# Optimization experiments

Measured on AMD Instinct MI355X. Metric: run time of the kernel, lower is better.

## Reference

```python
import jax, jax.numpy as jnp
import numpy as np

B, T, D = 2, 1024, 1024   # batch, seq, d_model
E, F = 8, 4096            # n_experts, expert hidden (4*d_model)


def setup_inputs() -> dict:
    key = jax.random.key(0)
    k1, k2, k3, k4, k5 = jax.random.split(key, 5)
    x = jax.random.normal(k1, (B, T, D), dtype=jnp.float32)
    token_mask = jax.random.randint(k2, (B, T), 0, 2).astype(jnp.int32)
    router_w = jax.random.normal(k3, (E, D), dtype=jnp.float32) * (1.0 / np.sqrt(D))
    w1 = jax.random.normal(k4, (E, D, F), dtype=jnp.float32) * (1.0 / np.sqrt(D))
    w2 = jax.random.normal(k5, (E, F, D), dtype=jnp.float32) * (1.0 / np.sqrt(F))
    return {"x": x, "token_mask": token_mask, "router_w": router_w, "w1": w1, "w2": w2}


def reference(x, token_mask, router_w, w1, w2):
    b, t, d = x.shape
    n_exp = router_w.shape[0]
    xf = x.reshape(b * t, d)                       # [N, D]
    # top-1 router
    logits = xf @ router_w.T                       # [N, E]
    probs = jax.nn.softmax(logits, axis=-1)
    expert_idx = jnp.argmax(probs, axis=-1)        # [N]
    gate = jnp.take_along_axis(probs, expert_idx[:, None], axis=1)[:, 0]  # [N]
    # expert FFNs: each token routed to exactly one expert (dense masked combine)
    y = jnp.zeros_like(xf)
    for e in range(n_exp):
        he = jnp.maximum(xf @ w1[e], 0.0) @ w2[e]  # [N, D]
        y = jnp.where(expert_idx[:, None] == e, he, y)
    # gate scaling + token masking (masked rows stay exactly zero,
    # matching torch's zero-init y_flat_all + index_copy_)
    mask = token_mask.reshape(b * t).astype(x.dtype)
    out = y * (gate * mask)[:, None]
    return out.reshape(b, t, d)
```

## Files before the change

kernel.cpp:

```cpp
#include <hip/hip_runtime.h>
#include <hip/hip_bf16.h>

#define NTOK 2048
#define DM 1024
#define NEXP 8
#define FFN 4096
#define BM 64
#define BN 64
#define BK 64
#define ASTR 72
#define MT1 8
#define G2_SPLIT 4

typedef __bf16 bf16x8 __attribute__((ext_vector_type(8)));
typedef __bf16 bf16x4 __attribute__((ext_vector_type(4)));
typedef float f32x4 __attribute__((ext_vector_type(4)));

__device__ __forceinline__ bf16x8 zero8() {
  bf16x8 z;
#pragma unroll
  for (int j = 0; j < 8; j++) z[j] = (__bf16)0.f;
  return z;
}

__device__ __forceinline__ void xpose4(float v[4], int quad) {
  const bool b0 = quad & 1;
  const bool b1 = (quad & 2) != 0;
  float t;
  t = __shfl_xor(b0 ? v[0] : v[1], 16, 64); if (b0) v[0] = t; else v[1] = t;
  t = __shfl_xor(b0 ? v[2] : v[3], 16, 64); if (b0) v[2] = t; else v[3] = t;
  t = __shfl_xor(b1 ? v[0] : v[2], 32, 64); if (b1) v[0] = t; else v[2] = t;
  t = __shfl_xor(b1 ? v[1] : v[3], 32, 64); if (b1) v[1] = t; else v[3] = t;
}

__device__ __forceinline__ bf16x8 readB(const char* BsB, int row, int kh, int quad) {
  return *(const bf16x8*)(BsB + row * 144 +
                          ((((kh << 2) + quad) ^ (row >> 3)) << 4));
}

#define STOREB(bb, v4, it) do {                                          \
    float vv[4] = {(v4).x, (v4).y, (v4).z, (v4).w};                      \
    xpose4(vv, quad);                                                    \
    bf16x4 o;                                                            \
    o[0] = (__bf16)vv[0]; o[1] = (__bf16)vv[1];                          \
    o[2] = (__bf16)vv[2]; o[3] = (__bf16)vv[3];                          \
    *(bf16x4*)((bb) + (((((it) << 1) + (w >> 1)) ^ rsw) << 4)) = o;      \
  } while (0)

__global__ __launch_bounds__(256) void router_gather(
    const float* __restrict__ x, const int* __restrict__ mask,
    const float* __restrict__ rw, int* __restrict__ counts,
    int* __restrict__ tlist, float* __restrict__ gateE,
    __bf16* __restrict__ xg)
{
  int wid = threadIdx.x >> 6, lane = threadIdx.x & 63;
  int t = blockIdx.x * 4 + wid;

  const float* xr = x + (size_t)t * DM;
  float xv[16];
#pragma unroll
  for (int i = 0; i < 4; i++) {
    const float4 v = *(const float4*)(xr + lane * 16 + i * 4);
    xv[i * 4 + 0] = v.x; xv[i * 4 + 1] = v.y;
    xv[i * 4 + 2] = v.z; xv[i * 4 + 3] = v.w;
  }

  float acc[NEXP];
#pragma unroll
  for (int e = 0; e < NEXP; e++) {
    float a = 0.f;
    const float* rwe = rw + e * DM + lane * 16;
#pragma unroll
    for (int i = 0; i < 4; i++) {
      const float4 r = *(const float4*)(rwe + i * 4);
      a += xv[i*4+0]*r.x + xv[i*4+1]*r.y + xv[i*4+2]*r.z + xv[i*4+3]*r.w;
    }
    acc[e] = a;
  }
#pragma unroll
  for (int e = 0; e < NEXP; e++)
#pragma unroll
    for (int s = 1; s < 64; s <<= 1) acc[e] += __shfl_xor(acc[e], s, 64);

  int pack = -1;
  if (lane == 0 && mask[t] != 0) {
    float m = acc[0]; int am = 0;
#pragma unroll
    for (int e = 1; e < NEXP; e++) if (acc[e] > m) { m = acc[e]; am = e; }
    float s = 0.f;
#pragma unroll
    for (int e = 0; e < NEXP; e++) s += __expf(acc[e] - m);
    int slot = atomicAdd(&counts[am], 1);
    tlist[am * NTOK + slot] = t;
    gateE[am * NTOK + slot] = 1.0f / s;
    pack = am * NTOK + slot;
  }
  pack = __shfl(pack, 0, 64);
  if (pack >= 0) {
    __bf16* dst = xg + (size_t)pack * DM + lane * 16;
    bf16x8 o0, o1;
#pragma unroll
    for (int j = 0; j < 8; j++) {
      o0[j] = (__bf16)xv[j];
      o1[j] = (__bf16)xv[8 + j];
    }
    *(bf16x8*)dst = o0;
    *(bf16x8*)(dst + 8) = o1;
  }
}

__global__ __launch_bounds__(256) void moe_gemm1(
    const __bf16* __restrict__ xg, const float* __restrict__ w1,
    const int* __restrict__ counts, const int* __restrict__ tlist,
    __bf16* __restrict__ h)
{
  int bx = blockIdx.x;
  int nt = bx & 63, mt = (bx >> 6) & (MT1 - 1), e = bx >> 9;
  int cnt = counts[e];
  if (mt * BM >= cnt) return;
  int n0 = nt * BN;

  __shared__ __bf16 As[BM][ASTR];
  __shared__ char   Bs[64 * 144];
  __shared__ int    toks[BM];

  int tid = threadIdx.x, lane = tid & 63, w = tid >> 6;
  int wm = w >> 1, wn = w & 1;
  int r16 = lane & 15, quad = lane >> 4;
  int rsw = r16 >> 1;
  char* bb = Bs + ((r16 << 2) + quad) * 144 + ((w & 1) << 3);

  const __bf16* xge = xg + (size_t)e * NTOK * DM;
  const float*  w1e = w1 + (size_t)e * DM * FFN;

  int ar = tid >> 2;
  int ak = (tid & 3) << 4;
  const float* bptr = w1e + (size_t)(w * 4 + quad) * FFN + n0 + (r16 << 2);

  bf16x8 a0r, a1r;
  float4 br0, br1, br2, br3;

#define LOADG1(kb) do {                                                   \
    a0r = av ? *(const bf16x8*)(aptr + (kb))     : zero8();               \
    a1r = av ? *(const bf16x8*)(aptr + (kb) + 8) : zero8();               \
    br0 = *(const float4*)(bptr + (size_t)((kb) +  0) * FFN);             \
    br1 = *(const float4*)(bptr + (size_t)((kb) + 16) * FFN);             \
    br2 = *(const float4*)(bptr + (size_t)((kb) + 32) * FFN);             \
    br3 = *(const float4*)(bptr + (size_t)((kb) + 48) * FFN);             \
  } while (0)

  for (int m0 = mt * BM; m0 < cnt; m0 += MT1 * BM) {
    bool av = (m0 + ar) < cnt;
    const __bf16* aptr = xge + (size_t)(m0 + ar) * DM + ak;

    f32x4 acc[2][2] = {};
    LOADG1(0);
    const int T = DM / BK;
    for (int t = 0; t < T; t++) {
      *(bf16x8*)&As[ar][ak]     = a0r;
      *(bf16x8*)&As[ar][ak + 8] = a1r;
      STOREB(bb, br0, 0); STOREB(bb, br1, 1); STOREB(bb, br2, 2); STOREB(bb, br3, 3);
      __syncthreads();
      if (t + 1 < T) LOADG1((t + 1) * BK);
#pragma unroll
      for (int kh = 0; kh < 2; kh++) {
        int ks = kh * 32 + (quad << 3);
        bf16x8 aA = *(const bf16x8*)&As[wm * 32 + r16][ks];
        bf16x8 aB = *(const bf16x8*)&As[wm * 32 + 16 + r16][ks];
        bf16x8 bA = readB(Bs, wn * 32 + r16, kh, quad);
        bf16x8 bB = readB(Bs, wn * 32 + 16 + r16, kh, quad);
        acc[0][0] = __builtin_amdgcn_mfma_f32_16x16x32_bf16(aA, bA, acc[0][0], 0, 0, 0);
        acc[0][1] = __builtin_amdgcn_mfma_f32_16x16x32_bf16(aA, bB, acc[0][1], 0, 0, 0);
        acc[1][0] = __builtin_amdgcn_mfma_f32_16x16x32_bf16(aB, bA, acc[1][0], 0, 0, 0);
        acc[1][1] = __builtin_amdgcn_mfma_f32_16x16x32_bf16(aB, bB, acc[1][1], 0, 0, 0);
      }
      __syncthreads();
    }

    if (tid < BM) toks[tid] = (m0 + tid < cnt) ? tlist[e * NTOK + m0 + tid] : -1;
    __syncthreads();

#pragma unroll
    for (int mf = 0; mf < 2; mf++) {
#pragma unroll
      for (int i = 0; i < 4; i++) {
        int row = wm * 32 + mf * 16 + (quad << 2) + i;
        int tok = toks[row];
        if (tok >= 0) {
          __bf16* hp = h + (size_t)tok * FFN + n0 + wn * 32 + r16;
          hp[0]  = (__bf16)fmaxf(acc[mf][0][i], 0.f);
          hp[16] = (__bf16)fmaxf(acc[mf][1][i], 0.f);
        }
      }
    }
    __syncthreads();
  }
#undef LOADG1
}

__global__ __launch_bounds__(256) void moe_gemm2(
    const __bf16* __restrict__ h, const float* __restrict__ w2,
    const int* __restrict__ counts, const int* __restrict__ tlist,
    const float* __restrict__ gateE, float* __restrict__ out)
{
  int bx = blockIdx.x;
  int nt = bx & 15, mt = (bx >> 4) & (MT1 - 1), e = (bx >> 7) & 7, sp = bx >> 10;
  int cnt = counts[e];
  if (mt * BM >= cnt) return;
  int n0 = nt * BN;
  int ksp = sp * (FFN / G2_SPLIT);

  __shared__ __bf16 As[BM][ASTR];
  __shared__ char   Bs[64 * 144];
  __shared__ int    toks[BM];
  __shared__ float  gts[BM];

  int tid = threadIdx.x, lane = tid & 63, w = tid >> 6;
  int wm = w >> 1, wn = w & 1;
  int r16 = lane & 15, quad = lane >> 4;
  int rsw = r16 >> 1;
  char* bb = Bs + ((r16 << 2) + quad) * 144 + ((w & 1) << 3);

  const float* w2e = w2 + (size_t)e * FFN * DM;
  int ar = tid >> 2;
  int ak = (tid & 3) << 4;
  const float* bptr = w2e + (size_t)(ksp + w * 4 + quad) * DM + n0 + (r16 << 2);

  bf16x8 a0r, a1r;
  float4 br0, br1, br2, br3;

#define LOADG2(kb) do {                                                   \
    a0r = av ? *(const bf16x8*)(aptr + (kb))     : zero8();               \
    a1r = av ? *(const bf16x8*)(aptr + (kb) + 8) : zero8();               \
    br0 = *(const float4*)(bptr + (size_t)((kb) +  0) * DM);              \
    br1 = *(const float4*)(bptr + (size_t)((kb) + 16) * DM);              \
    br2 = *(const float4*)(bptr + (size_t)((kb) + 32) * DM);              \
    br3 = *(const float4*)(bptr + (size_t)((kb) + 48) * DM);              \
  } while (0)

  for (int m0 = mt * BM; m0 < cnt; m0 += MT1 * BM) {
    if (tid < BM) {
      bool v = (m0 + tid) < cnt;
      toks[tid] = v ? tlist[e * NTOK + m0 + tid] : -1;
      gts[tid]  = v ? gateE[e * NTOK + m0 + tid] : 0.f;
    }
    __syncthreads();

    int tok0 = toks[ar];
    bool av = tok0 >= 0;
    const __bf16* aptr = h + (size_t)(av ? tok0 : 0) * FFN + ksp + ak;

    f32x4 acc[2][2] = {};
    LOADG2(0);
    const int T = (FFN / G2_SPLIT) / BK;
    for (int t = 0; t < T; t++) {
      *(bf16x8*)&As[ar][ak]     = a0r;
      *(bf16x8*)&As[ar][ak + 8] = a1r;
      STOREB(bb, br0, 0); STOREB(bb, br1, 1); STOREB(bb, br2, 2); STOREB(bb, br3, 3);
      __syncthreads();
      if (t + 1 < T) LOADG2((t + 1) * BK);
#pragma unroll
      for (int kh = 0; kh < 2; kh++) {
        int ks = kh * 32 + (quad << 3);
        bf16x8 aA = *(const bf16x8*)&As[wm * 32 + r16][ks];
        bf16x8 aB = *(const bf16x8*)&As[wm * 32 + 16 + r16][ks];
        bf16x8 bA = readB(Bs, wn * 32 + r16, kh, quad);
        bf16x8 bB = readB(Bs, wn * 32 + 16 + r16, kh, quad);
        acc[0][0] = __builtin_amdgcn_mfma_f32_16x16x32_bf16(aA, bA, acc[0][0], 0, 0, 0);
        acc[0][1] = __builtin_amdgcn_mfma_f32_16x16x32_bf16(aA, bB, acc[0][1], 0, 0, 0);
        acc[1][0] = __builtin_amdgcn_mfma_f32_16x16x32_bf16(aB, bA, acc[1][0], 0, 0, 0);
        acc[1][1] = __builtin_amdgcn_mfma_f32_16x16x32_bf16(aB, bB, acc[1][1], 0, 0, 0);
      }
      __syncthreads();
    }

#pragma unroll
    for (int mf = 0; mf < 2; mf++) {
#pragma unroll
      for (int i = 0; i < 4; i++) {
        int row = wm * 32 + mf * 16 + (quad << 2) + i;
        int tok = toks[row];
        if (tok >= 0) {
          float g = gts[row];
          float* op = out + (size_t)tok * DM + n0 + wn * 32 + r16;
          __hip_atomic_fetch_add(op, acc[mf][0][i] * g,
                                 __ATOMIC_RELAXED, __HIP_MEMORY_SCOPE_AGENT);
          __hip_atomic_fetch_add(op + 16, acc[mf][1][i] * g,
                                 __ATOMIC_RELAXED, __HIP_MEMORY_SCOPE_AGENT);
        }
      }
    }
    __syncthreads();
  }
#undef LOADG2
}

extern "C" void kernel_launch(void* const* d_in, const int* in_sizes, int n_in,
                              void* d_out, int out_size, void* d_ws, size_t ws_size,
                              hipStream_t stream) {
  const float* x    = (const float*)d_in[0];
  const int*   mask = (const int*)d_in[1];
  const float* rw   = (const float*)d_in[2];
  const float* w1   = (const float*)d_in[3];
  const float* w2   = (const float*)d_in[4];
  float* out = (float*)d_out;

  char* ws = (char*)d_ws;
  int*    counts = (int*)ws;
  int*    tlist  = (int*)(ws + 1024);
  float*  gateE  = (float*)(ws + 1024 + 65536);
  __bf16* xg     = (__bf16*)(ws + 132096);
  __bf16* h      = (__bf16*)(ws + 132096 +
                             (size_t)NEXP * NTOK * DM * 2);

  hipMemsetAsync(counts, 0, 1024, stream);
  hipMemsetAsync(out, 0, (size_t)out_size * sizeof(float), stream);

  router_gather<<<NTOK / 4, 256, 0, stream>>>(x, mask, rw, counts, tlist, gateE, xg);
  moe_gemm1<<<NEXP * MT1 * (FFN / BN), 256, 0, stream>>>(xg, w1, counts, tlist, h);
  moe_gemm2<<<G2_SPLIT * NEXP * MT1 * (DM / BN), 256, 0, stream>>>(
      h, w2, counts, tlist, gateE, out);
}
```

Baseline: 134.2 us.

## Double-buffer global prefetch and halve M-tile block count in MoE GEMMs

Both expert GEMMs now hold two register stages of global loads, so the tile for step t+2 is fetched while step t is stored to LDS and computed. Each kernel is unrolled by two over a fixed 16-step K loop. The number of M-tile slots per expert drops from 8 to 4, so each block loops over more row tiles and fewer blocks reload the same weight tile. Launch bounds now request 4 blocks per CU. The extra staging registers raise register pressure, and fewer blocks can reduce parallelism for experts that receive many tokens.

```diff
diff --git a/kernel.cpp b/kernel.cpp
--- a/kernel.cpp
+++ b/kernel.cpp
@@ -9,7 +9,7 @@
 #define BN 64
 #define BK 64
 #define ASTR 72
-#define MT1 8
+#define MTS 4
 #define G2_SPLIT 4
 
 typedef __bf16 bf16x8 __attribute__((ext_vector_type(8)));
@@ -109,13 +109,13 @@
   }
 }
 
-__global__ __launch_bounds__(256) void moe_gemm1(
+__global__ __launch_bounds__(256, 4) void moe_gemm1(
     const __bf16* __restrict__ xg, const float* __restrict__ w1,
     const int* __restrict__ counts, const int* __restrict__ tlist,
     __bf16* __restrict__ h)
 {
   int bx = blockIdx.x;
-  int nt = bx & 63, mt = (bx >> 6) & (MT1 - 1), e = bx >> 9;
+  int nt = bx & 63, mt = (bx >> 6) & (MTS - 1), e = bx >> 8;
   int cnt = counts[e];
   if (mt * BM >= cnt) return;
   int n0 = nt * BN;
@@ -137,44 +137,52 @@
   int ak = (tid & 3) << 4;
   const float* bptr = w1e + (size_t)(w * 4 + quad) * FFN + n0 + (r16 << 2);
 
-  bf16x8 a0r, a1r;
-  float4 br0, br1, br2, br3;
-
-#define LOADG1(kb) do {                                                   \
-    a0r = av ? *(const bf16x8*)(aptr + (kb))     : zero8();               \
-    a1r = av ? *(const bf16x8*)(aptr + (kb) + 8) : zero8();               \
-    br0 = *(const float4*)(bptr + (size_t)((kb) +  0) * FFN);             \
-    br1 = *(const float4*)(bptr + (size_t)((kb) + 16) * FFN);             \
-    br2 = *(const float4*)(bptr + (size_t)((kb) + 32) * FFN);             \
-    br3 = *(const float4*)(bptr + (size_t)((kb) + 48) * FFN);             \
-  } while (0)
-
-  for (int m0 = mt * BM; m0 < cnt; m0 += MT1 * BM) {
+  bf16x8 a0r[2], a1r[2];
+  float4 br[2][4];
+
+#define LOADG1(S, kb) do {                                                \
+    a0r[S] = av ? *(const bf16x8*)(aptr + (kb))     : zero8();            \
+    a1r[S] = av ? *(const bf16x8*)(aptr + (kb) + 8) : zero8();            \
+    br[S][0] = *(const float4*)(bptr + (size_t)((kb) +  0) * FFN);        \
+    br[S][1] = *(const float4*)(bptr + (size_t)((kb) + 16) * FFN);        \
+    br[S][2] = *(const float4*)(bptr + (size_t)((kb) + 32) * FFN);        \
+    br[S][3] = *(const float4*)(bptr + (size_t)((kb) + 48) * FFN);        \
+  } while (0)
+
+#define MFMA8() do {                                                      \
+    _Pragma("unroll") for (int kh = 0; kh < 2; kh++) {                    \
+      int ks = kh * 32 + (quad << 3);                                     \
+      bf16x8 aA = *(const bf16x8*)&As[wm * 32 + r16][ks];                 \
+      bf16x8 aB = *(const bf16x8*)&As[wm * 32 + 16 + r16][ks];            \
+      bf16x8 bA = readB(Bs, wn * 32 + r16, kh, quad);                     \
+      bf16x8 bB = readB(Bs, wn * 32 + 16 + r16, kh, quad);                \
+      acc[0][0] = __builtin_amdgcn_mfma_f32_16x16x32_bf16(aA, bA, acc[0][0], 0, 0, 0); \
+      acc[0][1] = __builtin_amdgcn_mfma_f32_16x16x32_bf16(aA, bB, acc[0][1], 0, 0, 0); \
+      acc[1][0] = __builtin_amdgcn_mfma_f32_16x16x32_bf16(aB, bA, acc[1][0], 0, 0, 0); \
+      acc[1][1] = __builtin_amdgcn_mfma_f32_16x16x32_bf16(aB, bB, acc[1][1], 0, 0, 0); \
+    } } while (0)
+
+#define STEP1(S, t) do {                                                  \
+    *(bf16x8*)&As[ar][ak]     = a0r[S];                                   \
+    *(bf16x8*)&As[ar][ak + 8] = a1r[S];                                   \
+    STOREB(bb, br[S][0], 0); STOREB(bb, br[S][1], 1);                     \
+    STOREB(bb, br[S][2], 2); STOREB(bb, br[S][3], 3);                     \
+    __syncthreads();                                                      \
+    if ((t) + 2 < 16) LOADG1(S, ((t) + 2) * BK);                          \
+    MFMA8();                                                              \
+    __syncthreads();                                                      \
+  } while (0)
+
+  for (int m0 = mt * BM; m0 < cnt; m0 += MTS * BM) {
     bool av = (m0 + ar) < cnt;
     const __bf16* aptr = xge + (size_t)(m0 + ar) * DM + ak;
 
     f32x4 acc[2][2] = {};
-    LOADG1(0);
-    const int T = DM / BK;
-    for (int t = 0; t < T; t++) {
-      *(bf16x8*)&As[ar][ak]     = a0r;
-      *(bf16x8*)&As[ar][ak + 8] = a1r;
-      STOREB(bb, br0, 0); STOREB(bb, br1, 1); STOREB(bb, br2, 2); STOREB(bb, br3, 3);
-      __syncthreads();
-      if (t + 1 < T) LOADG1((t + 1) * BK);
-#pragma unroll
-      for (int kh = 0; kh < 2; kh++) {
-        int ks = kh * 32 + (quad << 3);
-        bf16x8 aA = *(const bf16x8*)&As[wm * 32 + r16][ks];
-        bf16x8 aB = *(const bf16x8*)&As[wm * 32 + 16 + r16][ks];
-        bf16x8 bA = readB(Bs, wn * 32 + r16, kh, quad);
-        bf16x8 bB = readB(Bs, wn * 32 + 16 + r16, kh, quad);
-        acc[0][0] = __builtin_amdgcn_mfma_f32_16x16x32_bf16(aA, bA, acc[0][0], 0, 0, 0);
-        acc[0][1] = __builtin_amdgcn_mfma_f32_16x16x32_bf16(aA, bB, acc[0][1], 0, 0, 0);
-        acc[1][0] = __builtin_amdgcn_mfma_f32_16x16x32_bf16(aB, bA, acc[1][0], 0, 0, 0);
-        acc[1][1] = __builtin_amdgcn_mfma_f32_16x16x32_bf16(aB, bB, acc[1][1], 0, 0, 0);
-      }
-      __syncthreads();
+    LOADG1(0, 0);
+    LOADG1(1, BK);
+    for (int tt = 0; tt < 16; tt += 2) {
+      STEP1(0, tt);
+      STEP1(1, tt + 1);
     }
 
     if (tid < BM) toks[tid] = (m0 + tid < cnt) ? tlist[e * NTOK + m0 + tid] : -1;
@@ -195,16 +203,17 @@
     }
     __syncthreads();
   }
+#undef STEP1
 #undef LOADG1
 }
 
-__global__ __launch_bounds__(256) void moe_gemm2(
+__global__ __launch_bounds__(256, 4) void moe_gemm2(
     const __bf16* __restrict__ h, const float* __restrict__ w2,
     const int* __restrict__ counts, const int* __restrict__ tlist,
     const float* __restrict__ gateE, float* __restrict__ out)
 {
   int bx = blockIdx.x;
-  int nt = bx & 15, mt = (bx >> 4) & (MT1 - 1), e = (bx >> 7) & 7, sp = bx >> 10;
+  int nt = bx & 15, mt = (bx >> 4) & (MTS - 1), e = (bx >> 6) & 7, sp = bx >> 9;
   int cnt = counts[e];
   if (mt * BM >= cnt) return;
   int n0 = nt * BN;
@@ -226,19 +235,30 @@
   int ak = (tid & 3) << 4;
   const float* bptr = w2e + (size_t)(ksp + w * 4 + quad) * DM + n0 + (r16 << 2);
 
-  bf16x8 a0r, a1r;
-  float4 br0, br1, br2, br3;
-
-#define LOADG2(kb) do {                                                   \
-    a0r = av ? *(const bf16x8*)(aptr + (kb))     : zero8();               \
-    a1r = av ? *(const bf16x8*)(aptr + (kb) + 8) : zero8();               \
-    br0 = *(const float4*)(bptr + (size_t)((kb) +  0) * DM);              \
-    br1 = *(const float4*)(bptr + (size_t)((kb) + 16) * DM);              \
-    br2 = *(const float4*)(bptr + (size_t)((kb) + 32) * DM);              \
-    br3 = *(const float4*)(bptr + (size_t)((kb) + 48) * DM);              \
-  } while (0)
-
-  for (int m0 = mt * BM; m0 < cnt; m0 += MT1 * BM) {
+  bf16x8 a0r[2], a1r[2];
+  float4 br[2][4];
+
+#define LOADG2(S, kb) do {                                                \
+    a0r[S] = av ? *(const bf16x8*)(aptr + (kb))     : zero8();            \
+    a1r[S] = av ? *(const bf16x8*)(aptr + (kb) + 8) : zero8();            \
+    br[S][0] = *(const float4*)(bptr + (size_t)((kb) +  0) * DM);         \
+    br[S][1] = *(const float4*)(bptr + (size_t)((kb) + 16) * DM);         \
+    br[S][2] = *(const float4*)(bptr + (size_t)((kb) + 32) * DM);         \
+    br[S][3] = *(const float4*)(bptr + (size_t)((kb) + 48) * DM);         \
+  } while (0)
+
+#define STEP2(S, t) do {                                                  \
+    *(bf16x8*)&As[ar][ak]     = a0r[S];                                   \
+    *(bf16x8*)&As[ar][ak + 8] = a1r[S];                                   \
+    STOREB(bb, br[S][0], 0); STOREB(bb, br[S][1], 1);                     \
+    STOREB(bb, br[S][2], 2); STOREB(bb, br[S][3], 3);                     \
+    __syncthreads();                                                      \
+    if ((t) + 2 < 16) LOADG2(S, ((t) + 2) * BK);                          \
+    MFMA8();                                                              \
+    __syncthreads();                                                      \
+  } while (0)
+
+  for (int m0 = mt * BM; m0 < cnt; m0 += MTS * BM) {
     if (tid < BM) {
       bool v = (m0 + tid) < cnt;
       toks[tid] = v ? tlist[e * NTOK + m0 + tid] : -1;
@@ -251,27 +271,11 @@
     const __bf16* aptr = h + (size_t)(av ? tok0 : 0) * FFN + ksp + ak;
 
     f32x4 acc[2][2] = {};
-    LOADG2(0);
-    const int T = (FFN / G2_SPLIT) / BK;
-    for (int t = 0; t < T; t++) {
-      *(bf16x8*)&As[ar][ak]     = a0r;
-      *(bf16x8*)&As[ar][ak + 8] = a1r;
-      STOREB(bb, br0, 0); STOREB(bb, br1, 1); STOREB(bb, br2, 2); STOREB(bb, br3, 3);
-      __syncthreads();
-      if (t + 1 < T) LOADG2((t + 1) * BK);
-#pragma unroll
-      for (int kh = 0; kh < 2; kh++) {
-        int ks = kh * 32 + (quad << 3);
-        bf16x8 aA = *(const bf16x8*)&As[wm * 32 + r16][ks];
-        bf16x8 aB = *(const bf16x8*)&As[wm * 32 + 16 + r16][ks];
-        bf16x8 bA = readB(Bs, wn * 32 + r16, kh, quad);
-        bf16x8 bB = readB(Bs, wn * 32 + 16 + r16, kh, quad);
-        acc[0][0] = __builtin_amdgcn_mfma_f32_16x16x32_bf16(aA, bA, acc[0][0], 0, 0, 0);
-        acc[0][1] = __builtin_amdgcn_mfma_f32_16x16x32_bf16(aA, bB, acc[0][1], 0, 0, 0);
-        acc[1][0] = __builtin_amdgcn_mfma_f32_16x16x32_bf16(aB, bA, acc[1][0], 0, 0, 0);
-        acc[1][1] = __builtin_amdgcn_mfma_f32_16x16x32_bf16(aB, bB, acc[1][1], 0, 0, 0);
-      }
-      __syncthreads();
+    LOADG2(0, 0);
+    LOADG2(1, BK);
+    for (int tt = 0; tt < 16; tt += 2) {
+      STEP2(0, tt);
+      STEP2(1, tt + 1);
     }
 
 #pragma unroll
@@ -292,6 +296,7 @@
     }
     __syncthreads();
   }
+#undef STEP2
 #undef LOADG2
 }
 
@@ -317,7 +322,7 @@
   hipMemsetAsync(out, 0, (size_t)out_size * sizeof(float), stream);
 
   router_gather<<<NTOK / 4, 256, 0, stream>>>(x, mask, rw, counts, tlist, gateE, xg);
-  moe_gemm1<<<NEXP * MT1 * (FFN / BN), 256, 0, stream>>>(xg, w1, counts, tlist, h);
-  moe_gemm2<<<G2_SPLIT * NEXP * MT1 * (DM / BN), 256, 0, stream>>>(
+  moe_gemm1<<<NEXP * MTS * (FFN / BN), 256, 0, stream>>>(xg, w1, counts, tlist, h);
+  moe_gemm2<<<G2_SPLIT * NEXP * MTS * (DM / BN), 256, 0, stream>>>(
       h, w2, counts, tlist, gateE, out);
 }
```

Measured after the change: 171.5 us. 27.8% more time.
